# Performance work log

Hardware: AMD Instinct MI355X
Metric: run time of the kernel (lower is better)

## Reference

```python
import jax, jax.numpy as jnp
import numpy as np

B, T, S, H, V = 4, 512, 1024, 768, 50257

def setup_inputs() -> dict:
    key = jax.random.key(0)
    k1, k2, k3, k4, k5, k6 = jax.random.split(key, 6)
    input_ids_to_copy = jax.random.randint(k1, (B, S), 0, V)
    cross_attentions = jax.random.uniform(k2, (B, T, S), dtype=jnp.float32)
    # normalize like attention weights
    cross_attentions = cross_attentions / jnp.sum(cross_attentions, axis=-1, keepdims=True)
    src_hidden_states = jax.random.normal(k3, (B, S, H), dtype=jnp.float32)
    tgt_hidden_states = jax.random.normal(k4, (B, T, H), dtype=jnp.float32)
    # p_gen_head = Linear(2H, 1) + Sigmoid
    W_pgen = jax.random.normal(k5, (2 * H, 1), dtype=jnp.float32) * (1.0 / np.sqrt(2 * H))
    b_pgen = jnp.zeros((1,), dtype=jnp.float32)
    return {
        "input_ids_to_copy": input_ids_to_copy,
        "cross_attentions": cross_attentions,
        "src_hidden_states": src_hidden_states,
        "tgt_hidden_states": tgt_hidden_states,
        "W_pgen": W_pgen,
        "b_pgen": b_pgen,
    }

def _copy_logits(attn_bts, ids_bs, vocab_size):
    # logits[b,t,v] = sum_s attn[b,t,s] * (ids[b,s] == v)
    # Efficient scatter-add over source positions instead of one-hot + matmul.
    def per_batch(attn_ts, ids_s):
        # attn_ts: [T,S], ids_s: [S] -> segment_sum over S -> [V,T] -> [T,V]
        return jax.ops.segment_sum(attn_ts.T, ids_s, num_segments=vocab_size).T
    return jax.vmap(per_batch)(attn_bts, ids_bs)

def reference(input_ids_to_copy, cross_attentions, src_hidden_states,
              tgt_hidden_states, W_pgen, b_pgen):
    # context_vectors: [B,T,H]
    context_vectors = jnp.einsum('bts,bsh->bth', cross_attentions, src_hidden_states)
    total_states = jnp.concatenate((context_vectors, tgt_hidden_states), axis=-1)  # [B,T,2H]
    p_gen = jax.nn.sigmoid(total_states @ W_pgen + b_pgen)  # [B,T,1]
    logits = _copy_logits(cross_attentions, input_ids_to_copy, V)  # [B,T,V]
    return (p_gen, logits)
```

## Files before the change

### kernel.cpp

```cpp
#include <hip/hip_runtime.h>
#include <hip/hip_bf16.h>
#include <math.h>

#define BB 4
#define TT 512
#define SS 1024
#define HH 768
#define VV 50257
#define NW 1571
#define CHUNK 2048
#define NCH 25

__global__ __launch_bounds__(256) void proj_kernel(
    const float* __restrict__ src, const float* __restrict__ tgt,
    const float* __restrict__ W, const float* __restrict__ bptr,
    float* __restrict__ src_proj, float* __restrict__ tgt_proj)
{
    const int wave = threadIdx.x >> 6;
    const int lane = threadIdx.x & 63;
    const int row  = blockIdx.x * 4 + wave;

    const float* vec;
    const float* w;
    if (row < BB * SS) { vec = src + (size_t)row * HH;            w = W; }
    else               { vec = tgt + (size_t)(row - BB*SS) * HH;  w = W + HH; }
    const float4* v4 = (const float4*)vec;
    const float4* w4 = (const float4*)w;

    float acc = 0.f;
#pragma unroll
    for (int k = 0; k < 3; ++k) {
        float4 a = v4[k * 64 + lane];
        float4 b = w4[k * 64 + lane];
        acc += a.x * b.x + a.y * b.y + a.z * b.z + a.w * b.w;
    }
#pragma unroll
    for (int off = 32; off > 0; off >>= 1) acc += __shfl_down(acc, off);
    if (lane == 0) {
        if (row < BB * SS) src_proj[row] = acc;
        else               tgt_proj[row - BB * SS] = acc + bptr[0];
    }
}

__global__ __launch_bounds__(256) void batch_setup(
    const int* __restrict__ ids,
    unsigned short* __restrict__ rank_g,
    unsigned short* __restrict__ col_g)
{
    __shared__ unsigned bm[NW];
    __shared__ unsigned pre[NW];
    __shared__ unsigned scan[256];
    __shared__ unsigned short coll[SS];
    const int b = blockIdx.x, tid = threadIdx.x;

    for (int i = tid; i < NW; i += 256) bm[i] = 0u;
    for (int i = tid; i < SS; i += 256) coll[i] = 0xFFFFu;
    __syncthreads();
    const int* idb = ids + b * SS;
    for (int s = tid; s < SS; s += 256) {
        const int v = idb[s];
        atomicOr(&bm[v >> 5], 1u << (v & 31));
    }
    __syncthreads();

    unsigned cnt[7];
    unsigned local = 0;
    const int w0 = tid * 7;
#pragma unroll
    for (int k = 0; k < 7; ++k) {
        const int w = w0 + k;
        cnt[k] = local;
        local += (w < NW) ? (unsigned)__popc(bm[w]) : 0u;
    }
    scan[tid] = local;
    __syncthreads();
    for (int off = 1; off < 256; off <<= 1) {
        const unsigned mine = scan[tid];
        const unsigned add  = (tid >= off) ? scan[tid - off] : 0u;
        __syncthreads();
        scan[tid] = mine + add;
        __syncthreads();
    }
    const unsigned excl = (tid > 0) ? scan[tid - 1] : 0u;
#pragma unroll
    for (int k = 0; k < 7; ++k) {
        const int w = w0 + k;
        if (w < NW) pre[w] = excl + cnt[k];
    }
    __syncthreads();
    for (int s = tid; s < SS; s += 256) {
        const int v = idb[s];
        const unsigned w = (unsigned)v >> 5, bit = (unsigned)v & 31u;
        const unsigned r = pre[w] + (unsigned)__popc(bm[w] & ((1u << bit) - 1u));
        rank_g[b * SS + s] = (unsigned short)r;
        coll[r] = (unsigned short)v;
    }
    __syncthreads();
    for (int i = tid; i < SS; i += 256) col_g[b * SS + i] = coll[i];
}

__global__ __launch_bounds__(256) void row_kernel(
    const float* __restrict__ attn,
    const float* __restrict__ src_proj,
    const float* __restrict__ tgt_proj,
    const unsigned short* __restrict__ rank_g,
    const unsigned short* __restrict__ col_g,
    float* __restrict__ out)
{
    __shared__ unsigned short col[SS];
    __shared__ float vals[SS];
    __shared__ int bnd[NCH + 1];
    __shared__ float wsum[4];

    const int row = blockIdx.x;
    const int b   = row >> 9;
    const int tid = threadIdx.x;

    for (int i = tid; i < SS; i += 256) { col[i] = col_g[b * SS + i]; vals[i] = 0.f; }
    __syncthreads();

    const float4*  a4p = (const float4*)(attn + (size_t)row * SS);
    const float4*  sp4 = (const float4*)(src_proj + b * SS);
    const ushort4* r4p = (const ushort4*)(rank_g + b * SS);
    const float4  a = a4p[tid];
    const float4  p = sp4[tid];
    const ushort4 r = r4p[tid];
    atomicAdd(&vals[r.x], a.x);
    atomicAdd(&vals[r.y], a.y);
    atomicAdd(&vals[r.z], a.z);
    atomicAdd(&vals[r.w], a.w);
    float acc = a.x * p.x + a.y * p.y + a.z * p.z + a.w * p.w;

    if (tid <= NCH) {
        const unsigned short key = (unsigned short)(tid * CHUNK);
        int lo = 0, hi = SS;
        while (lo < hi) {
            const int mid = (lo + hi) >> 1;
            if (col[mid] < key) lo = mid + 1; else hi = mid;
        }
        bnd[tid] = lo;
    }

#pragma unroll
    for (int off = 32; off > 0; off >>= 1) acc += __shfl_down(acc, off);
    if ((tid & 63) == 0) wsum[tid >> 6] = acc;
    __syncthreads();
    if (tid == 0) {
        const float x = wsum[0] + wsum[1] + wsum[2] + wsum[3] + tgt_proj[row];
        out[row] = 1.f / (1.f + expf(-x));
    }

    float* logits = out + (BB * TT) + (size_t)row * VV;
    const int head = (int)(((16u - (unsigned)((uintptr_t)logits & 15u)) & 15u) >> 2);
    const float4 z4 = make_float4(0.f, 0.f, 0.f, 0.f);

    for (int c = 0; c < NCH; ++c) {
        const int lo = c * CHUNK;
        const int hi = (lo + CHUNK < VV) ? lo + CHUNK : VV;
        if (tid < head) logits[lo + tid] = 0.f;
        const int n4 = (hi - lo - head) >> 2;
        float4* p4 = (float4*)(logits + lo + head);
        for (int i = tid; i < n4; i += 256) p4[i] = z4;
        for (int v = lo + head + (n4 << 2) + tid; v < hi; v += 256) logits[v] = 0.f;
        __syncthreads();
        for (int idx = bnd[c] + tid; idx < bnd[c + 1]; idx += 256)
            logits[col[idx]] = vals[idx];
    }
}

extern "C" void kernel_launch(void* const* d_in, const int* in_sizes, int n_in,
                              void* d_out, int out_size, void* d_ws, size_t ws_size,
                              hipStream_t stream) {
    const int*   ids  = (const int*)d_in[0];
    const float* attn = (const float*)d_in[1];
    const float* src  = (const float*)d_in[2];
    const float* tgt  = (const float*)d_in[3];
    const float* W    = (const float*)d_in[4];
    const float* bp   = (const float*)d_in[5];

    float* out = (float*)d_out;

    float*          src_proj = (float*)d_ws;
    float*          tgt_proj = src_proj + BB * SS;
    unsigned short* rank_g   = (unsigned short*)(tgt_proj + BB*TT);
    unsigned short* col_g    = rank_g + BB * SS;

    proj_kernel<<<(BB * SS + BB * TT) / 4, 256, 0, stream>>>(
        src, tgt, W, bp, src_proj, tgt_proj);
    batch_setup<<<BB, 256, 0, stream>>>(ids, rank_g, col_g);
    row_kernel<<<BB * TT, 256, 0, stream>>>(
        attn, src_proj, tgt_proj, rank_g, col_g, out);
}
```

Before: 468.6 us.

## Split copy-logit scatter into compact vals pass and coalesced gather fill

The per-row kernel previously zero-filled each 50257-wide logits row in chunks, synchronised, and then scattered nonzero values into the same memory. It now runs in two stages. One kernel accumulates each row's compacted attention sums into a global buffer. A grid-stride kernel then writes every logits float4 exactly once, using the per-batch bitmap and prefix counts to gather any nonzero entries. This removes the double writes, the per-chunk barriers and the binary searches, at the cost of an extra 8 MB round trip through global memory and an integer division per float4.

New measurement: 546.9 us. 16.7% more time.

```diff
diff --git a/kernel.cpp b/kernel.cpp
--- a/kernel.cpp
+++ b/kernel.cpp
@@ -8,8 +8,8 @@
 #define HH 768
 #define VV 50257
 #define NW 1571
-#define CHUNK 2048
-#define NCH 25
+#define NWP 1600
+#define NF4 25731584u
 
 __global__ __launch_bounds__(256) void proj_kernel(
     const float* __restrict__ src, const float* __restrict__ tgt,
@@ -44,17 +44,16 @@
 
 __global__ __launch_bounds__(256) void batch_setup(
     const int* __restrict__ ids,
-    unsigned short* __restrict__ rank_g,
-    unsigned short* __restrict__ col_g)
+    unsigned* __restrict__ bm_g,
+    unsigned* __restrict__ pre_g,
+    unsigned short* __restrict__ rank_g)
 {
     __shared__ unsigned bm[NW];
     __shared__ unsigned pre[NW];
     __shared__ unsigned scan[256];
-    __shared__ unsigned short coll[SS];
     const int b = blockIdx.x, tid = threadIdx.x;
 
     for (int i = tid; i < NW; i += 256) bm[i] = 0u;
-    for (int i = tid; i < SS; i += 256) coll[i] = 0xFFFFu;
     __syncthreads();
     const int* idb = ids + b * SS;
     for (int s = tid; s < SS; s += 256) {
@@ -85,7 +84,12 @@
 #pragma unroll
     for (int k = 0; k < 7; ++k) {
         const int w = w0 + k;
-        if (w < NW) pre[w] = excl + cnt[k];
+        if (w < NW) {
+            const unsigned p = excl + cnt[k];
+            pre[w] = p;
+            pre_g[b * NWP + w] = p;
+            bm_g[b * NWP + w]  = bm[w];
+        }
     }
     __syncthreads();
     for (int s = tid; s < SS; s += 256) {
@@ -93,30 +97,24 @@
         const unsigned w = (unsigned)v >> 5, bit = (unsigned)v & 31u;
         const unsigned r = pre[w] + (unsigned)__popc(bm[w] & ((1u << bit) - 1u));
         rank_g[b * SS + s] = (unsigned short)r;
-        coll[r] = (unsigned short)v;
-    }
-    __syncthreads();
-    for (int i = tid; i < SS; i += 256) col_g[b * SS + i] = coll[i];
-}
-
-__global__ __launch_bounds__(256) void row_kernel(
+    }
+}
+
+__global__ __launch_bounds__(256) void vals_kernel(
     const float* __restrict__ attn,
     const float* __restrict__ src_proj,
     const float* __restrict__ tgt_proj,
     const unsigned short* __restrict__ rank_g,
-    const unsigned short* __restrict__ col_g,
+    float* __restrict__ vals_g,
     float* __restrict__ out)
 {
-    __shared__ unsigned short col[SS];
     __shared__ float vals[SS];
-    __shared__ int bnd[NCH + 1];
     __shared__ float wsum[4];
-
     const int row = blockIdx.x;
     const int b   = row >> 9;
     const int tid = threadIdx.x;
 
-    for (int i = tid; i < SS; i += 256) { col[i] = col_g[b * SS + i]; vals[i] = 0.f; }
+    ((float4*)vals)[tid] = make_float4(0.f, 0.f, 0.f, 0.f);
     __syncthreads();
 
     const float4*  a4p = (const float4*)(attn + (size_t)row * SS);
@@ -130,17 +128,6 @@
     atomicAdd(&vals[r.z], a.z);
     atomicAdd(&vals[r.w], a.w);
     float acc = a.x * p.x + a.y * p.y + a.z * p.z + a.w * p.w;
-
-    if (tid <= NCH) {
-        const unsigned short key = (unsigned short)(tid * CHUNK);
-        int lo = 0, hi = SS;
-        while (lo < hi) {
-            const int mid = (lo + hi) >> 1;
-            if (col[mid] < key) lo = mid + 1; else hi = mid;
-        }
-        bnd[tid] = lo;
-    }
-
 #pragma unroll
     for (int off = 32; off > 0; off >>= 1) acc += __shfl_down(acc, off);
     if ((tid & 63) == 0) wsum[tid >> 6] = acc;
@@ -149,22 +136,67 @@
         const float x = wsum[0] + wsum[1] + wsum[2] + wsum[3] + tgt_proj[row];
         out[row] = 1.f / (1.f + expf(-x));
     }
-
-    float* logits = out + (BB * TT) + (size_t)row * VV;
-    const int head = (int)(((16u - (unsigned)((uintptr_t)logits & 15u)) & 15u) >> 2);
-    const float4 z4 = make_float4(0.f, 0.f, 0.f, 0.f);
-
-    for (int c = 0; c < NCH; ++c) {
-        const int lo = c * CHUNK;
-        const int hi = (lo + CHUNK < VV) ? lo + CHUNK : VV;
-        if (tid < head) logits[lo + tid] = 0.f;
-        const int n4 = (hi - lo - head) >> 2;
-        float4* p4 = (float4*)(logits + lo + head);
-        for (int i = tid; i < n4; i += 256) p4[i] = z4;
-        for (int v = lo + head + (n4 << 2) + tid; v < hi; v += 256) logits[v] = 0.f;
-        __syncthreads();
-        for (int idx = bnd[c] + tid; idx < bnd[c + 1]; idx += 256)
-            logits[col[idx]] = vals[idx];
+    ((float4*)(vals_g + (size_t)row * SS))[tid] = ((const float4*)vals)[tid];
+}
+
+__device__ __forceinline__ float lutg(unsigned row, unsigned col,
+                                      const unsigned* __restrict__ bm_g,
+                                      const unsigned* __restrict__ pre_g,
+                                      const float* __restrict__ vals_g)
+{
+    const unsigned b = row >> 9;
+    const unsigned w = bm_g[b * NWP + (col >> 5)];
+    const unsigned bit = col & 31u;
+    if ((w >> bit) & 1u) {
+        const unsigned r = pre_g[b * NWP + (col >> 5)]
+                         + (unsigned)__popc(w & ((1u << bit) - 1u));
+        return vals_g[(size_t)row * SS + r];
+    }
+    return 0.f;
+}
+
+__global__ __launch_bounds__(256) void fillsub_kernel(
+    const unsigned* __restrict__ bm_g,
+    const unsigned* __restrict__ pre_g,
+    const float* __restrict__ vals_g,
+    float* __restrict__ logits)
+{
+    const unsigned G = gridDim.x * 256u;
+    float4* p4 = (float4*)logits;
+    for (unsigned f = blockIdx.x * 256u + threadIdx.x; f < NF4; f += G) {
+        const unsigned elem = f << 2;
+        const unsigned row  = elem / VV;
+        const unsigned col  = elem - row * VV;
+        float4 o = make_float4(0.f, 0.f, 0.f, 0.f);
+        if (col + 3u < VV) {
+            const unsigned b  = row >> 9;
+            const unsigned wi = col >> 5;
+            const unsigned w  = bm_g[b * NWP + wi];
+            const unsigned sh = col & 31u;
+            unsigned nib;
+            if (sh <= 28u) {
+                nib = (w >> sh) & 0xFu;
+            } else {
+                const unsigned w2 = bm_g[b * NWP + wi + 1];
+                nib = ((w >> sh) | (w2 << (32u - sh))) & 0xFu;
+            }
+            if (nib) {
+                if (nib & 1u) o.x = lutg(row, col,      bm_g, pre_g, vals_g);
+                if (nib & 2u) o.y = lutg(row, col + 1u, bm_g, pre_g, vals_g);
+                if (nib & 4u) o.z = lutg(row, col + 2u, bm_g, pre_g, vals_g);
+                if (nib & 8u) o.w = lutg(row, col + 3u, bm_g, pre_g, vals_g);
+            }
+        } else {
+            unsigned e0 = elem;
+            float* oo = &o.x;
+#pragma unroll
+            for (int e = 0; e < 4; ++e) {
+                const unsigned re = (e0 + e) / VV;
+                const unsigned ce = (e0 + e) - re * VV;
+                oo[e] = lutg(re, ce, bm_g, pre_g, vals_g);
+            }
+        }
+        p4[f] = o;
     }
 }
 
@@ -182,12 +214,16 @@
 
     float*          src_proj = (float*)d_ws;
     float*          tgt_proj = src_proj + BB * SS;
-    unsigned short* rank_g   = (unsigned short*)(tgt_proj + BB*TT);
-    unsigned short* col_g    = rank_g + BB * SS;
+    float*          vals_g   = tgt_proj + BB * TT;
+    unsigned*       bm_g     = (unsigned*)(vals_g + (size_t)BB*TT*SS);
+    unsigned*       pre_g    = bm_g + BB * NWP;
+    unsigned short* rank_g   = (unsigned short*)(pre_g + BB * NWP);
 
     proj_kernel<<<(BB * SS + BB * TT) / 4, 256, 0, stream>>>(
         src, tgt, W, bp, src_proj, tgt_proj);
-    batch_setup<<<BB, 256, 0, stream>>>(ids, rank_g, col_g);
-    row_kernel<<<BB * TT, 256, 0, stream>>>(
-        attn, src_proj, tgt_proj, rank_g, col_g, out);
-}
+    batch_setup<<<BB, 256, 0, stream>>>(ids, bm_g, pre_g, rank_g);
+    vals_kernel<<<BB * TT, 256, 0, stream>>>(
+        attn, src_proj, tgt_proj, rank_g, vals_g, out);
+    fillsub_kernel<<<1024, 256, 0, stream>>>(
+        bm_g, pre_g, vals_g, out + BB * TT);
+}
```
